# Optimization experiments

Hardware: AMD Instinct MI355X
Metric: run time of the kernel (lower is better)

The kernel has to match this reference:

```python
import jax, jax.numpy as jnp
import numpy as np

N = 250_000    # total nodes across the batch of graphs
E = 2_000_000  # directed edges (no self loops)
F_IN = 3       # PROTEINS node feature dim
H = 32         # hid_channel
B = 128        # number of graphs in the batch


def _connected_components(u, v, n):
    """Weakly-connected components over selected edges via min-label propagation
    with pointer jumping. Final label = min node id in the component."""
    lab0 = jnp.arange(n, dtype=u.dtype)
    def body(state):
        lab, _ = state
        m = jnp.minimum(lab[u], lab[v])
        new = lab.at[u].min(m).at[v].min(m)
        new = jnp.minimum(new, new[new])  # pointer jumping
        return new, jnp.any(new != lab)
    lab, _ = jax.lax.while_loop(lambda s: s[1], body, (lab0, jnp.bool_(True)))
    return lab


def _gcn(h, src, dst, w, self_w, n):
    """GCN propagation D^-1/2 (A + I) D^-1/2 h with per-edge weights w and
    per-node self-loop weights self_w (gcn_norm with add_remaining_self_loops)."""
    deg = jax.ops.segment_sum(w, dst, num_segments=n) + self_w
    dis = jnp.where(deg > 0, jax.lax.rsqrt(jnp.maximum(deg, 1e-12)), 0.0)
    msg = jax.ops.segment_sum(h[src] * (dis[src] * dis[dst] * w)[:, None], dst, num_segments=n)
    return msg + h * (dis * dis * self_w)[:, None]


def _forward(x, W1, b1, w_pool, b_pool, W3, b3, Wf, bf, src, dst, batch):
    n = x.shape[0]
    ew = jnp.ones_like(src, dtype=x.dtype)
    sw = jnp.ones((n,), x.dtype)
    # conv1 + ReLU (dropout = identity in eval mode)
    x1 = jax.nn.relu(_gcn(x @ W1, src, dst, ew, sw, n) + b1)
    # ClusterPooling edge scores: sigmoid(Linear([x_i ; x_j]))
    h = x1.shape[1]
    score = jax.nn.sigmoid(x1[src] @ w_pool[:h] + x1[dst] @ w_pool[h:] + b_pool)
    sel = score > 0.5
    # contract selected edges -> clusters (unselected edges mapped to harmless (0,0))
    u = jax.lax.stop_gradient(jnp.where(sel, src, 0))
    v = jax.lax.stop_gradient(jnp.where(sel, dst, 0))
    lab = _connected_components(u, v, n)            # cluster id = representative (min) node id
    rep = lab == jnp.arange(n, dtype=lab.dtype)     # valid (non-empty) cluster slots
    repf = rep.astype(x.dtype)
    # cluster score = mean score of contracted edges; 1.0 for singleton clusters
    grp = lab[src]
    cnt = jax.ops.segment_sum(sel.astype(x.dtype), grp, num_segments=n)
    ssum = jax.ops.segment_sum(jnp.where(sel, score, jnp.zeros_like(score)), grp, num_segments=n)
    cscore = jnp.where(cnt > 0, ssum / jnp.maximum(cnt, 1.0), 1.0)
    # new cluster features = (sum of member features) * cluster score
    new_x = jax.ops.segment_sum(x1, lab, num_segments=n) * cscore[:, None]
    # relabel edges to cluster ids, coalesce (dedup) and drop self loops
    ru, rv = lab[src], lab[dst]
    order = jnp.lexsort((rv, ru))
    rus, rvs = ru[order], rv[order]
    first = jnp.concatenate([jnp.ones((1,), bool), (rus[1:] != rus[:-1]) | (rvs[1:] != rvs[:-1])])
    w = (first & (rus != rvs)).astype(x.dtype)
    # conv3 + ReLU on pooled graph (self loops only on valid cluster slots)
    x3 = jax.nn.relu(_gcn(new_x @ W3, rus, rvs, w, repf, n) + b3)
    # global mean pool over the clusters of each graph (invalid slots -> dummy seg B)
    seg = jnp.where(rep, batch, B)
    gs = jax.ops.segment_sum(x3 * repf[:, None], seg, num_segments=B + 1)[:B]
    gc = jax.ops.segment_sum(repf, seg, num_segments=B + 1)[:B]
    pooled = gs / jnp.maximum(gc, 1.0)[:, None]
    return jax.nn.sigmoid(pooled @ Wf + bf).reshape(-1)  # [B], binary task -> sigmoid + flatten


def setup_inputs() -> dict:
    key = jax.random.key(0)
    ks = jax.random.split(key, 10)
    x = jax.random.normal(ks[0], (N, F_IN), dtype=jnp.float32)
    src = jax.random.randint(ks[1], (E,), 0, N, dtype=jnp.int32)
    off = jax.random.randint(ks[2], (E,), 1, N, dtype=jnp.int32)
    dst = ((src + off) % N).astype(jnp.int32)  # no self loops
    edge_list = jnp.stack([src, dst], axis=1)  # [E, 2], forward transposes
    batch = jnp.sort(jax.random.randint(ks[3], (N,), 0, B, dtype=jnp.int32))
    W1 = jax.random.normal(ks[4], (F_IN, H), jnp.float32) * 0.5
    b1 = jnp.zeros((H,), jnp.float32)
    w_pool = jax.random.normal(ks[5], (2 * H,), jnp.float32) * 0.5
    b_pool = jnp.float32(-1.0)
    W3 = jax.random.normal(ks[6], (H, H), jnp.float32) * 0.3
    b3 = jnp.zeros((H,), jnp.float32)
    Wf = jax.random.normal(ks[7], (H, 1), jnp.float32) * 0.3
    bf = jnp.zeros((1,), jnp.float32)
    return dict(x=x, edge_list=edge_list, batch=batch, W1=W1, b1=b1,
                w_pool=w_pool, b_pool=b_pool, W3=W3, b3=b3, Wf=Wf, bf=bf)


def reference(x, edge_list, batch, W1, b1, w_pool, b_pool, W3, b3, Wf, bf):
    src, dst = edge_list[:, 0], edge_list[:, 1]
    return _forward(x, W1, b1, w_pool, b_pool, W3, b3, Wf, bf, src, dst, batch)
```

## Files before the change

kernel.cpp:

```cpp
#include <hip/hip_runtime.h>

typedef unsigned long long u64;
typedef unsigned int u32;

#define HF 32
#define TBL_BITS 22
#define TBL_SIZE (1u << TBL_BITS)
#define LP_ITERS 12
#define EMPTY_KEY 0xFFFFFFFFFFFFFFFFull
#define HSLOTS 256


__global__ void k_count(const int2* __restrict__ edges, int* __restrict__ cnt, int E) {
    int e = blockIdx.x * blockDim.x + threadIdx.x;
    if (e >= E) return;
    atomicAdd(&cnt[edges[e].y], 1);
}

__global__ void k_scan1(const int* __restrict__ cnt, int* __restrict__ row,
                        int* __restrict__ bsums, int N) {
    __shared__ int s[256];
    int tid = threadIdx.x;
    int i = blockIdx.x * 256 + tid;
    int v = (i < N) ? cnt[i] : 0;
    s[tid] = v;
    __syncthreads();
    for (int o = 1; o < 256; o <<= 1) {
        int t = (tid >= o) ? s[tid - o] : 0;
        __syncthreads();
        s[tid] += t;
        __syncthreads();
    }
    if (i < N) row[i] = s[tid] - v;
    if (tid == 255) bsums[blockIdx.x] = s[255];
}

__global__ void k_scan2(int* __restrict__ bsums, int nb) {
    __shared__ int s[1024];
    int tid = threadIdx.x;
    int v = (tid < nb) ? bsums[tid] : 0;
    s[tid] = v;
    __syncthreads();
    for (int o = 1; o < 1024; o <<= 1) {
        int t = (tid >= o) ? s[tid - o] : 0;
        __syncthreads();
        s[tid] += t;
        __syncthreads();
    }
    if (tid < nb) bsums[tid] = s[tid] - v;
}

__global__ void k_scan3(int* __restrict__ row, int* __restrict__ cursor,
                        const int* __restrict__ bsums, int N, int E) {
    int i = blockIdx.x * 256 + threadIdx.x;
    if (i < N) {
        int v = row[i] + bsums[blockIdx.x];
        row[i] = v;
        cursor[i] = v;
    }
    if (i == 0) row[N] = E;
}

__global__ void k_fill(const int2* __restrict__ edges, int* __restrict__ cursor,
                       int* __restrict__ csr_src, int E, int N) {
    int xcd = blockIdx.x & 7;
    int nlo = (int)((long long)N * xcd >> 3);
    int nhi = (int)((long long)N * (xcd + 1) >> 3);
    int nblk = gridDim.x >> 3;
    int bslot = blockIdx.x >> 3;
    int stride = nblk * 256;
    for (int e = bslot * 256 + threadIdx.x; e < E; e += stride) {
        int2 ed = edges[e];
        if (ed.y >= nlo && ed.y < nhi) {
            int pos = atomicAdd(&cursor[ed.y], 1);
            csr_src[pos] = ed.x;
        }
    }
}


__global__ void k_gather_x1(const int* __restrict__ row, const int* __restrict__ csr_src,
                            const float* __restrict__ x, const float* __restrict__ W1,
                            const float* __restrict__ b1, const float* __restrict__ wp,
                            float* __restrict__ x1, float* __restrict__ a_src,
                            float* __restrict__ a_dst, int* __restrict__ lab, int N) {
    __shared__ float w[96];
    __shared__ float wpl[64];
    __shared__ float b1l[32];
    int tid = threadIdx.x;
    if (tid < 96) w[tid] = W1[tid];
    if (tid < 64) wpl[tid] = wp[tid];
    if (tid < 32) b1l[tid] = b1[tid];
    __syncthreads();
    int t = blockIdx.x * blockDim.x + tid;
    int i = t >> 3, fg = t & 7;
    if (i >= N) return;
    int f = fg * 4;
    float wa0 = w[f + 0], wa1 = w[f + 1], wa2 = w[f + 2], wa3 = w[f + 3];
    float wb0 = w[32 + f + 0], wb1 = w[32 + f + 1], wb2 = w[32 + f + 2], wb3 = w[32 + f + 3];
    float wc0 = w[64 + f + 0], wc1 = w[64 + f + 1], wc2 = w[64 + f + 2], wc3 = w[64 + f + 3];
    int r0 = row[i], r1 = row[i + 1];
    float disI = rsqrtf((float)(r1 - r0) + 1.0f);
    float xi0 = x[3 * i + 0], xi1 = x[3 * i + 1], xi2 = x[3 * i + 2];
    float4 acc;
    acc.x = (xi0 * wa0 + xi1 * wb0 + xi2 * wc0) * disI;
    acc.y = (xi0 * wa1 + xi1 * wb1 + xi2 * wc1) * disI;
    acc.z = (xi0 * wa2 + xi1 * wb2 + xi2 * wc2) * disI;
    acc.w = (xi0 * wa3 + xi1 * wb3 + xi2 * wc3) * disI;
    for (int j = r0; j < r1; j++) {
        int s = csr_src[j];
        float s0 = x[3 * s + 0], s1 = x[3 * s + 1], s2 = x[3 * s + 2];
        int sr0 = row[s], sr1 = row[s + 1];
        float disS = rsqrtf((float)(sr1 - sr0) + 1.0f);
        acc.x += (s0 * wa0 + s1 * wb0 + s2 * wc0) * disS;
        acc.y += (s0 * wa1 + s1 * wb1 + s2 * wc1) * disS;
        acc.z += (s0 * wa2 + s1 * wb2 + s2 * wc2) * disS;
        acc.w += (s0 * wa3 + s1 * wb3 + s2 * wc3) * disS;
    }
    float4 r;
    r.x = fmaxf(disI * acc.x + b1l[f + 0], 0.0f);
    r.y = fmaxf(disI * acc.y + b1l[f + 1], 0.0f);
    r.z = fmaxf(disI * acc.z + b1l[f + 2], 0.0f);
    r.w = fmaxf(disI * acc.w + b1l[f + 3], 0.0f);
    ((float4*)x1)[i * 8 + fg] = r;
    float ps = r.x * wpl[f + 0] + r.y * wpl[f + 1] + r.z * wpl[f + 2] + r.w * wpl[f + 3];
    float pd = r.x * wpl[32 + f + 0] + r.y * wpl[32 + f + 1] + r.z * wpl[32 + f + 2] + r.w * wpl[32 + f + 3];
#pragma unroll
    for (int o = 4; o; o >>= 1) {
        ps += __shfl_xor(ps, o);
        pd += __shfl_xor(pd, o);
    }
    if (fg == 0) {
        a_src[i] = ps;
        a_dst[i] = pd;
        lab[i] = i;
    }
}


__global__ void k_select(const int2* __restrict__ edges, const float* __restrict__ a_src,
                         const float* __restrict__ a_dst, const float* __restrict__ bp,
                         long long* __restrict__ seluv, float* __restrict__ selsc,
                         int* __restrict__ selcnt, int E) {
    __shared__ int wsum[4];
    __shared__ int sbase;
    int tid = threadIdx.x;
    int e = blockIdx.x * 256 + tid;
    bool sel = false;
    long long pk = 0;
    float score = 0.0f;
    if (e < E) {
        int2 ed = edges[e];
        float z = a_src[ed.x] + a_dst[ed.y] + bp[0];
        score = 1.0f / (1.0f + expf(-z));
        if (score > 0.5f) {
            sel = true;
            pk = ((long long)ed.x << 32) | (u32)ed.y;
        }
    }
    u64 m = __ballot(sel);
    int wid = tid >> 6, lane = tid & 63;
    if (lane == 0) wsum[wid] = __popcll(m);
    __syncthreads();
    if (tid == 0) {
        int tot = wsum[0] + wsum[1] + wsum[2] + wsum[3];
        sbase = tot ? atomicAdd(selcnt, tot) : 0;
    }
    __syncthreads();
    if (sel) {
        int woff = 0;
        for (int k = 0; k < wid; k++) woff += wsum[k];
        int rank = __popcll(m & ((1ull << lane) - 1ull));
        int pos = sbase + woff + rank;
        seluv[pos] = pk;
        selsc[pos] = score;
    }
}


__global__ void k_lp(const long long* __restrict__ seluv, const int* __restrict__ pcnt,
                     int* __restrict__ lab, int* __restrict__ flags, int t, int N) {
    if (t > 0 && flags[t - 1] == 0) return;
    int n = *pcnt;
    int ch = 0;
    int tid0 = blockIdx.x * blockDim.x + threadIdx.x;
    int stride = gridDim.x * blockDim.x;
    for (int idx = tid0; idx < n; idx += stride) {
        long long pk = seluv[idx];
        int u = (int)(pk >> 32), v = (int)(u32)pk;
        int lu = lab[u], lv = lab[v];
        if (lu < lv) { atomicMin(&lab[v], lu); ch = 1; }
        else if (lv < lu) { atomicMin(&lab[u], lv); ch = 1; }
    }
    for (int i = tid0; i < N; i += stride) {
        int l = lab[i];
        int m = lab[l];
        int m2 = lab[m];
        if (m2 < l) { atomicMin(&lab[i], m2); ch = 1; }
    }
    if (__ballot(ch) && (int)(threadIdx.x & 63) == 0) flags[t] = 1;
}


__global__ void k_cnt_ssum(const long long* __restrict__ seluv, const float* __restrict__ selsc,
                           const int* __restrict__ pcnt, const int* __restrict__ lab,
                           float* __restrict__ cnt, float* __restrict__ ssum) {
    __shared__ int hkey[HSLOTS];
    __shared__ float hcnt[HSLOTS];
    __shared__ float hsum[HSLOTS];
    int tid = threadIdx.x;
    for (int k = tid; k < HSLOTS; k += 256) {
        hkey[k] = -1;
        hcnt[k] = 0.0f;
        hsum[k] = 0.0f;
    }
    __syncthreads();
    int n = *pcnt;
    for (int base = blockIdx.x * blockDim.x; base < n; base += gridDim.x * blockDim.x) {
        int idx = base + tid;
        bool valid = idx < n;
        int g = -1;
        float score = 0.0f;
        if (valid) {
            long long pk = seluv[idx];
            int s = (int)(pk >> 32);
            score = selsc[idx];
            g = lab[s];
        }
        u64 m = __ballot(valid);
        while (m) {
            int leader = __ffsll(m) - 1;
            int g0 = __shfl(g, leader);
            bool match = valid && (g == g0);
            float c = match ? 1.0f : 0.0f;
            float sv = match ? score : 0.0f;
#pragma unroll
            for (int o = 32; o; o >>= 1) {
                c += __shfl_xor(c, o);
                sv += __shfl_xor(sv, o);
            }
            if ((int)(tid & 63) == leader) {
                u32 h = ((u32)g0 * 0x9E3779B9u) >> 24;
                bool done = false;
                for (int probe = 0; probe < 16; probe++) {
                    int k = (int)((h + probe) & (HSLOTS - 1));
                    int prev = atomicCAS(&hkey[k], -1, g0);
                    if (prev == -1 || prev == g0) {
                        atomicAdd(&hcnt[k], c);
                        atomicAdd(&hsum[k], sv);
                        done = true;
                        break;
                    }
                }
                if (!done) {
                    atomicAdd(&cnt[g0], c);
                    atomicAdd(&ssum[g0], sv);
                }
            }
            m &= ~__ballot(match);
        }
    }
    __syncthreads();
    for (int k = tid; k < HSLOTS; k += 256) {
        int g = hkey[k];
        if (g >= 0) {
            atomicAdd(&cnt[g], hcnt[k]);
            atomicAdd(&ssum[g], hsum[k]);
        }
    }
}

__global__ void k_findgl(const float* __restrict__ cnt, u64* __restrict__ glpack, int N) {
    int i = blockIdx.x * blockDim.x + threadIdx.x;
    u64 v = 0;
    if (i < N) v = ((u64)__float_as_uint(cnt[i]) << 32) | (u32)i;
#pragma unroll
    for (int o = 32; o; o >>= 1) {
        u64 ov = __shfl_xor(v, o);
        v = v > ov ? v : ov;
    }
    if ((int)(threadIdx.x & 63) == 0) {
        if (*glpack < v) atomicMax(glpack, v);
    }
}

__global__ void k_nx_scatter(const float* __restrict__ x1, const int* __restrict__ lab,
                             const u64* __restrict__ glpack, float* __restrict__ nx, int N) {
    __shared__ float ls[HF];
    int tid = threadIdx.x;
    if (tid < HF) ls[tid] = 0.0f;
    __syncthreads();
    int gl = (int)(u32)(*glpack);
    int t = blockIdx.x * blockDim.x + tid;
    int i = t >> 3, fg = t & 7;
    if (i < N) {
        int l = lab[i];
        float4 v = ((const float4*)x1)[i * 8 + fg];
        if (l == gl) {
            atomicAdd(&ls[fg * 4 + 0], v.x);
            atomicAdd(&ls[fg * 4 + 1], v.y);
            atomicAdd(&ls[fg * 4 + 2], v.z);
            atomicAdd(&ls[fg * 4 + 3], v.w);
        } else {
            float* d = &nx[l * HF + fg * 4];
            atomicAdd(d + 0, v.x);
            atomicAdd(d + 1, v.y);
            atomicAdd(d + 2, v.z);
            atomicAdd(d + 3, v.w);
        }
    }
    __syncthreads();
    if (tid < HF) {
        float s = ls[tid];
        if (s != 0.0f) atomicAdd(&nx[gl * HF + tid], s);
    }
}


__global__ void k_hash_insert(const int2* __restrict__ edges, const int* __restrict__ lab,
                              u64* __restrict__ htab, float* __restrict__ deg3, int E) {
    int e = blockIdx.x * blockDim.x + threadIdx.x;
    if (e >= E) return;
    int2 ed = edges[e];
    int ru = lab[ed.x];
    int rv = lab[ed.y];
    if (ru == rv) return;
    u64 key = ((u64)(u32)ru << 32) | (u32)rv;
    u32 slot = (u32)((key * 0x9E3779B97F4A7C15ull) >> (64 - TBL_BITS));
    bool won = false;
    for (;;) {
        u64 cur = htab[slot];
        if (cur == key) break;
        if (cur == EMPTY_KEY) {
            u64 prev = atomicCAS(&htab[slot], EMPTY_KEY, key);
            if (prev == EMPTY_KEY) { won = true; break; }
            if (prev == key) break;
        }
        slot = (slot + 1) & (TBL_SIZE - 1);
    }
    if (won) atomicAdd(&deg3[rv], 1.0f);
}

__global__ void k_h3(const float* __restrict__ nx, const float* __restrict__ cnt,
                     const float* __restrict__ ssum, const float* __restrict__ deg3,
                     const int* __restrict__ lab, const float* __restrict__ W3,
                     float* __restrict__ hs3, float* __restrict__ dis3, int N) {
    __shared__ float w[HF * HF];
    int tid = threadIdx.x;
    for (int k = tid; k < HF * HF; k += blockDim.x) w[k] = W3[k];
    __syncthreads();
    int i = blockIdx.x * blockDim.x + tid;
    if (i >= N) return;
    if (lab[i] != i) {
        dis3[i] = 0.0f;
        return;
    }
    float cn = cnt[i];
    float c = cn > 0.0f ? ssum[i] / fmaxf(cn, 1.0f) : 1.0f;
    float d3 = 1.0f / sqrtf(deg3[i] + 1.0f);
    dis3[i] = d3;
    float scale = c * d3;
    float r[HF];
#pragma unroll
    for (int f = 0; f < HF; f++) r[f] = 0.0f;
    for (int k = 0; k < HF; k++) {
        float xv = nx[i * HF + k];
#pragma unroll
        for (int f = 0; f < HF; f++) r[f] += xv * w[k * HF + f];
    }
#pragma unroll
    for (int f = 0; f < HF; f++) hs3[i * HF + f] = r[f] * scale;
}

__global__ void k_hash_scatter(const u64* __restrict__ htab, const float* __restrict__ hs3,
                               float* __restrict__ acc3, const u64* __restrict__ glpack) {
    __shared__ float ls[HF];
    int tid = threadIdx.x;
    if (tid < HF) ls[tid] = 0.0f;
    __syncthreads();
    int gl = (int)(u32)(*glpack);
    int t = blockIdx.x * blockDim.x + tid;
    u32 slot = (u32)(t >> 3);
    int fg = t & 7;
    u64 key = htab[slot];
    if (key != EMPTY_KEY) {
        int a = (int)(key >> 32), b = (int)(u32)key;
        float4 v = ((const float4*)hs3)[a * 8 + fg];
        if (b == gl) {
            atomicAdd(&ls[fg * 4 + 0], v.x);
            atomicAdd(&ls[fg * 4 + 1], v.y);
            atomicAdd(&ls[fg * 4 + 2], v.z);
            atomicAdd(&ls[fg * 4 + 3], v.w);
        } else {
            float* d = &acc3[b * HF + fg * 4];
            atomicAdd(d + 0, v.x);
            atomicAdd(d + 1, v.y);
            atomicAdd(d + 2, v.z);
            atomicAdd(d + 3, v.w);
        }
    }
    __syncthreads();
    if (tid < HF) {
        float s = ls[tid];
        if (s != 0.0f) atomicAdd(&acc3[gl * HF + tid], s);
    }
}

__global__ void k_final(const float* __restrict__ acc3, const float* __restrict__ hs3,
                        const float* __restrict__ dis3, const int* __restrict__ lab,
                        const int* __restrict__ batch, const float* __restrict__ b3,
                        float* __restrict__ gs, float* __restrict__ gc, int N) {
    int t = blockIdx.x * blockDim.x + threadIdx.x;
    int i = t >> 3, fg = t & 7;
    if (i >= N) return;
    if (lab[i] != i) return;
    float d3 = dis3[i];
    float4 a = ((const float4*)acc3)[i * 8 + fg];
    float4 h = ((const float4*)hs3)[i * 8 + fg];
    int f = fg * 4;
    float4 x3;
    x3.x = fmaxf(d3 * (a.x + h.x) + b3[f + 0], 0.0f);
    x3.y = fmaxf(d3 * (a.y + h.y) + b3[f + 1], 0.0f);
    x3.z = fmaxf(d3 * (a.z + h.z) + b3[f + 2], 0.0f);
    x3.w = fmaxf(d3 * (a.w + h.w) + b3[f + 3], 0.0f);
    int b = batch[i];
    float* g = &gs[b * HF + f];
    atomicAdd(g + 0, x3.x);
    atomicAdd(g + 1, x3.y);
    atomicAdd(g + 2, x3.z);
    atomicAdd(g + 3, x3.w);
    if (fg == 0) atomicAdd(&gc[b], 1.0f);
}

__global__ void k_out(const float* __restrict__ gs, const float* __restrict__ gc,
                      const float* __restrict__ Wf, const float* __restrict__ bf,
                      float* __restrict__ out, int B) {
    int b = threadIdx.x + blockIdx.x * blockDim.x;
    if (b >= B) return;
    float inv = 1.0f / fmaxf(gc[b], 1.0f);
    float z = 0.0f;
#pragma unroll
    for (int f = 0; f < HF; f++) z += gs[b * HF + f] * inv * Wf[f];
    z += bf[0];
    out[b] = 1.0f / (1.0f + expf(-z));
}


static inline size_t align256(size_t x) { return (x + 255) & ~(size_t)255; }

extern "C" void kernel_launch(void* const* d_in, const int* in_sizes, int n_in,
                              void* d_out, int out_size, void* d_ws, size_t ws_size,
                              hipStream_t stream) {
    const float* x = (const float*)d_in[0];
    const int2* edges = (const int2*)d_in[1];
    const int* batch = (const int*)d_in[2];
    const float* W1 = (const float*)d_in[3];
    const float* b1 = (const float*)d_in[4];
    const float* wp = (const float*)d_in[5];
    const float* bp = (const float*)d_in[6];
    const float* W3 = (const float*)d_in[7];
    const float* b3 = (const float*)d_in[8];
    const float* Wf = (const float*)d_in[9];
    const float* bf = (const float*)d_in[10];
    float* outp = (float*)d_out;

    const int N = in_sizes[2];
    const int E = in_sizes[1] / 2;
    const int B = out_size;

    char* p = (char*)d_ws;
    size_t off = 0;
    auto alloc = [&](size_t bytes) -> void* {
        void* r = p + off;
        off = align256(off + bytes);
        return r;
    };
    float* f0 = (float*)alloc((size_t)N * HF * 4);
    float* f1 = (float*)alloc((size_t)N * HF * 4);
    int* row = (int*)alloc((size_t)(N + 1) * 4);
    int* cursor = (int*)alloc((size_t)N * 4);
    int* bsums = (int*)alloc(4096);
    int* csr_src = (int*)alloc((size_t)E * 4);
    float* a_src = (float*)alloc((size_t)N * 4);
    float* a_dst = (float*)alloc((size_t)N * 4);
    int* lab = (int*)alloc((size_t)N * 4);
    float* cnt = (float*)alloc((size_t)N * 4);
    float* ssum = (float*)alloc((size_t)N * 4);
    float* deg3 = (float*)alloc((size_t)N * 4);
    float* dis3 = (float*)alloc((size_t)N * 4);
    long long* seluv = (long long*)alloc((size_t)E * 8);
    float* selsc = (float*)alloc((size_t)E * 4);
    int* selcnt = (int*)alloc(4);
    int* flags = (int*)alloc(LP_ITERS * 4);
    u64* glpack = (u64*)alloc(8);
    float* gs = (float*)alloc((size_t)B * HF * 4);
    float* gc = (float*)alloc((size_t)B * 4);
    u64* htab = (u64*)alloc((size_t)TBL_SIZE * 8);
    (void)ws_size; (void)n_in;

    const int nb_e = (E + 255) / 256;
    const int nb_n8 = (int)(((size_t)N * 8 + 255) / 256);
    const int nb_n = (N + 255) / 256;
    const int nb_tbl8 = (int)(((size_t)TBL_SIZE * 8) / 256);

    hipMemsetAsync(cursor, 0, (size_t)N * 4, stream);
    hipMemsetAsync(cnt, 0, (size_t)N * 4, stream);
    hipMemsetAsync(ssum, 0, (size_t)N * 4, stream);
    hipMemsetAsync(selcnt, 0, 4, stream);
    hipMemsetAsync(deg3, 0, (size_t)N * 4, stream);
    hipMemsetAsync(flags, 0, LP_ITERS * 4, stream);
    hipMemsetAsync(glpack, 0, 8, stream);
    hipMemsetAsync(gs, 0, (size_t)B * HF * 4, stream);
    hipMemsetAsync(gc, 0, (size_t)B * 4, stream);
    hipMemsetAsync(htab, 0xFF, (size_t)TBL_SIZE * 8, stream);

    k_count<<<nb_e, 256, 0, stream>>>(edges, cursor, E);
    k_scan1<<<nb_n, 256, 0, stream>>>(cursor, row, bsums, N);
    k_scan2<<<1, 1024, 0, stream>>>(bsums, nb_n);
    k_scan3<<<nb_n, 256, 0, stream>>>(row, cursor, bsums, N, E);
    k_fill<<<2048, 256, 0, stream>>>(edges, cursor, csr_src, E, N);

    k_gather_x1<<<nb_n8, 256, 0, stream>>>(row, csr_src, x, W1, b1, wp, f1, a_src, a_dst, lab, N);

    k_select<<<nb_e, 256, 0, stream>>>(edges, a_src, a_dst, bp, seluv, selsc, selcnt, E);
    for (int t = 0; t < LP_ITERS; t++) {
        k_lp<<<2048, 256, 0, stream>>>(seluv, selcnt, lab, flags, t, N);
    }

    k_cnt_ssum<<<1024, 256, 0, stream>>>(seluv, selsc, selcnt, lab, cnt, ssum);
    k_findgl<<<nb_n, 256, 0, stream>>>(cnt, glpack, N);
    hipMemsetAsync(f0, 0, (size_t)N * HF * 4, stream);
    k_nx_scatter<<<nb_n8, 256, 0, stream>>>(f1, lab, glpack, f0, N);

    k_hash_insert<<<nb_e, 256, 0, stream>>>(edges, lab, htab, deg3, E);
    k_h3<<<nb_n, 256, 0, stream>>>(f0, cnt, ssum, deg3, lab, W3, f1, dis3, N);
    hipMemsetAsync(f0, 0, (size_t)N * HF * 4, stream);
    k_hash_scatter<<<nb_tbl8, 256, 0, stream>>>(htab, f1, f0, glpack);
    k_final<<<nb_n8, 256, 0, stream>>>(f0, f1, dis3, lab, batch, b3, gs, gc, N);
    k_out<<<1, 128, 0, stream>>>(gs, gc, Wf, bf, outp, B);
}
```

Measured before the change: 997.3 us.

## Use shrinking edge frontier in label propagation and hook labels during selection

Each label-propagation pass now compacts the edges that still changed a label into a ping-pong frontier buffer, so later passes only visit active edges instead of all selected edges. Edge selection also does a first hooking step on the labels while it already holds the endpoints. This is meant to cut the repeated full scans of the selected-edge list. In exchange it adds block-level ballot compaction with extra barriers, a per-iteration counter memset, and two extra edge-sized buffers. Dropping edges whose endpoints already share a label relies on pointer jumping to carry later label decreases, which could weaken convergence within the fixed iteration cap.

```diff
diff --git a/kernel.cpp b/kernel.cpp
--- a/kernel.cpp
+++ b/kernel.cpp
@@ -141,7 +141,7 @@
 __global__ void k_select(const int2* __restrict__ edges, const float* __restrict__ a_src,
                          const float* __restrict__ a_dst, const float* __restrict__ bp,
                          long long* __restrict__ seluv, float* __restrict__ selsc,
-                         int* __restrict__ selcnt, int E) {
+                         int* __restrict__ selcnt, int* __restrict__ lab, int E) {
     __shared__ int wsum[4];
     __shared__ int sbase;
     int tid = threadIdx.x;
@@ -156,6 +156,9 @@
         if (score > 0.5f) {
             sel = true;
             pk = ((long long)ed.x << 32) | (u32)ed.y;
+            int lu = lab[ed.x], lv = lab[ed.y];
+            if (lu < lv) atomicMin(&lab[ed.y], lu);
+            else if (lv < lu) atomicMin(&lab[ed.x], lv);
         }
     }
     u64 m = __ballot(sel);
@@ -178,27 +181,52 @@
 }
 
 
-__global__ void k_lp(const long long* __restrict__ seluv, const int* __restrict__ pcnt,
+__global__ void k_lp(const long long* __restrict__ frsrc, const int* __restrict__ pcsrc,
+                     long long* __restrict__ frdst, int* __restrict__ pcdst,
                      int* __restrict__ lab, int* __restrict__ flags, int t, int N) {
     if (t > 0 && flags[t - 1] == 0) return;
-    int n = *pcnt;
+    __shared__ int wsum[4];
+    __shared__ int sbase;
+    int n = *pcsrc;
+    int tid = threadIdx.x;
+    int wid = tid >> 6, lane = tid & 63;
     int ch = 0;
-    int tid0 = blockIdx.x * blockDim.x + threadIdx.x;
+    for (int base = blockIdx.x * 256; base < n; base += gridDim.x * 256) {
+        int idx = base + tid;
+        bool keep = false;
+        long long pk = 0;
+        if (idx < n) {
+            pk = frsrc[idx];
+            int u = (int)(pk >> 32), v = (int)(u32)pk;
+            int lu = lab[u], lv = lab[v];
+            if (lu < lv) { atomicMin(&lab[v], lu); keep = true; ch = 1; }
+            else if (lv < lu) { atomicMin(&lab[u], lv); keep = true; ch = 1; }
+        }
+        u64 m = __ballot(keep);
+        if (lane == 0) wsum[wid] = __popcll(m);
+        __syncthreads();
+        if (tid == 0) {
+            int tot = wsum[0] + wsum[1] + wsum[2] + wsum[3];
+            sbase = tot ? atomicAdd(pcdst, tot) : 0;
+        }
+        __syncthreads();
+        if (keep) {
+            int woff = 0;
+            for (int k = 0; k < wid; k++) woff += wsum[k];
+            int rank = __popcll(m & ((1ull << lane) - 1ull));
+            frdst[sbase + woff + rank] = pk;
+        }
+        __syncthreads();
+    }
+    int tid0 = blockIdx.x * blockDim.x + tid;
     int stride = gridDim.x * blockDim.x;
-    for (int idx = tid0; idx < n; idx += stride) {
-        long long pk = seluv[idx];
-        int u = (int)(pk >> 32), v = (int)(u32)pk;
-        int lu = lab[u], lv = lab[v];
-        if (lu < lv) { atomicMin(&lab[v], lu); ch = 1; }
-        else if (lv < lu) { atomicMin(&lab[u], lv); ch = 1; }
-    }
     for (int i = tid0; i < N; i += stride) {
         int l = lab[i];
         int m = lab[l];
         int m2 = lab[m];
         if (m2 < l) { atomicMin(&lab[i], m2); ch = 1; }
     }
-    if (__ballot(ch) && (int)(threadIdx.x & 63) == 0) flags[t] = 1;
+    if (__ballot(ch) && lane == 0) flags[t] = 1;
 }
 
 
@@ -490,6 +518,9 @@
     float* dis3 = (float*)alloc((size_t)N * 4);
     long long* seluv = (long long*)alloc((size_t)E * 8);
     float* selsc = (float*)alloc((size_t)E * 4);
+    long long* frB = (long long*)alloc((size_t)E * 8);
+    long long* frC = (long long*)alloc((size_t)E * 8);
+    int* fc = (int*)alloc(8);
     int* selcnt = (int*)alloc(4);
     int* flags = (int*)alloc(LP_ITERS * 4);
     u64* glpack = (u64*)alloc(8);
@@ -522,9 +553,14 @@
 
     k_gather_x1<<<nb_n8, 256, 0, stream>>>(row, csr_src, x, W1, b1, wp, f1, a_src, a_dst, lab, N);
 
-    k_select<<<nb_e, 256, 0, stream>>>(edges, a_src, a_dst, bp, seluv, selsc, selcnt, E);
+    k_select<<<nb_e, 256, 0, stream>>>(edges, a_src, a_dst, bp, seluv, selsc, selcnt, lab, E);
     for (int t = 0; t < LP_ITERS; t++) {
-        k_lp<<<2048, 256, 0, stream>>>(seluv, selcnt, lab, flags, t, N);
+        const long long* src = (t == 0) ? seluv : ((t & 1) ? frB : frC);
+        const int* srcc = (t == 0) ? selcnt : &fc[(t + 1) & 1];
+        long long* dst = (t & 1) ? frC : frB;
+        int* dstc = &fc[t & 1];
+        hipMemsetAsync(dstc, 0, 4, stream);
+        k_lp<<<2048, 256, 0, stream>>>(src, srcc, dst, dstc, lab, flags, t, N);
     }
 
     k_cnt_ssum<<<1024, 256, 0, stream>>>(seluv, selsc, selcnt, lab, cnt, ssum);
```

New measurement: 2.610 ms. 2.62x slower.
